# Kernel tuning notes

Measured on AMD Instinct MI355X. Metric: run time of the kernel, lower is better.

Reference implementation:

```python
import jax, jax.numpy as jnp
import numpy as np


def setup_inputs() -> dict:
    key = jax.random.key(0)
    ks = jax.random.split(key, 8)
    E = 2_000_000          # num facts (edges)
    B, M = 8, 2000         # batch, max_local_entity -> B*M = 16000 entity slots
    R, D = 2000, 128       # num relations, hidden size (in_features == out_features)
    return {
        "local_entity": jax.random.randint(ks[0], (B, M), 0, M),
        "batch_heads": jax.random.randint(ks[1], (E,), 0, B * M),
        "batch_tails": jax.random.randint(ks[2], (E,), 0, B * M),
        "batch_rels": jax.random.randint(ks[3], (E,), 0, R),
        "val_one": jax.random.uniform(ks[4], (E,), dtype=jnp.float32),
        "rel_features": jax.random.normal(ks[5], (R, D), dtype=jnp.float32),
        "W": jax.random.normal(ks[6], (D, D), dtype=jnp.float32) * 0.05,
        "b": jax.random.normal(ks[7], (D,), dtype=jnp.float32) * 0.05,
    }


def reference(local_entity, batch_heads, batch_tails, batch_rels, val_one,
              rel_features, W, b):
    B, M = local_entity.shape
    num_ent = B * M
    # gather relation features per fact, linear transform (nn.Linear: x @ W.T + b)
    fact_rel = rel_features[batch_rels]            # [E, D]
    fact_val = fact_rel @ W.T + b                  # [E, D]
    # sparse COO mm == weighted scatter-add of fact_val into entity slots
    weighted = fact_val * val_one[:, None]         # [E, D]
    tail_agg = jax.ops.segment_sum(weighted, batch_tails, num_segments=num_ent)
    head_agg = jax.ops.segment_sum(weighted, batch_heads, num_segments=num_ent)
    f2e_emb = jax.nn.relu(tail_agg + head_agg)     # [B*M, D]
    return f2e_emb.reshape(B, M, -1)
```

## Files before the change

kernel.cpp:

```cpp
#include <hip/hip_runtime.h>
#include <hip/hip_bf16.h>
#include <cstdint>

typedef _Float16 half2v __attribute__((ext_vector_type(2)));

#define EPB   16
#define MAXNB 1024
#define FPB   4096
#define FPT   16
#define SORTCAP 4608
#define CPT   9

__global__ void rwb_row_kernel(const float* __restrict__ rel, const float* __restrict__ W,
                               const float* __restrict__ b, _Float16* __restrict__ rwb,
                               int R) {
    const int k = blockIdx.x;
    const int n = threadIdx.x;
    __shared__ float relk[128];
    relk[n] = rel[(size_t)k * 128 + n];
    __syncthreads();
    const float4* w4 = reinterpret_cast<const float4*>(W + (size_t)n * 128);
    const float4* r4 = reinterpret_cast<const float4*>(relk);
    float acc = 0.f;
#pragma unroll
    for (int i = 0; i < 32; ++i) {
        float4 a = r4[i], w = w4[i];
        acc += a.x * w.x + a.y * w.y + a.z * w.z + a.w * w.w;
    }
    rwb[(size_t)k * 128 + n] = (_Float16)(acc + b[n]);
}

__device__ __noinline__ void spill_add(float* __restrict__ out, const _Float16* __restrict__ rwb,
                                       int v, int r, float val) {
    float* o = out + (size_t)v * 128;
    const _Float16* rw = rwb + (size_t)r * 128;
    for (int n = 0; n < 128; ++n) unsafeAtomicAdd(o + n, val * (float)rw[n]);
}

__global__ __launch_bounds__(256) void bin_kernel(
    const int* __restrict__ heads, const int* __restrict__ tails,
    const int* __restrict__ rels, const float* __restrict__ val,
    int* __restrict__ gcnt, uint2* __restrict__ slots,
    const _Float16* __restrict__ rwb, float* __restrict__ out,
    int E, int NB, int CAPB) {
    __shared__ int cnt[MAXNB];
    __shared__ int gbase[MAXNB];
    const int t = threadIdx.x;
    for (int k = t; k < NB; k += 256) cnt[k] = 0;
    __syncthreads();

    const int base = blockIdx.x * FPB;
    unsigned keyT[FPT], keyH[FPT], prT[FPT], prH[FPT];
    float fv[FPT];
#pragma unroll
    for (int u = 0; u < FPT; ++u) {
        const int i = base + u * 256 + t;
        prT[u] = 0xFFFFFFFFu;
        prH[u] = 0xFFFFFFFFu;
        if (i < E) {
            const int tl = tails[i], hd = heads[i], r = rels[i];
            fv[u] = val[i];
            const int bt = tl >> 4, bh = hd >> 4;
            keyT[u] = ((unsigned)(tl & 15) << 24) | (unsigned)r;
            keyH[u] = ((unsigned)(hd & 15) << 24) | (unsigned)r;
            const int rt = atomicAdd(&cnt[bt], 1);
            const int rh = atomicAdd(&cnt[bh], 1);
            prT[u] = ((unsigned)bt << 16) | (unsigned)rt;
            prH[u] = ((unsigned)bh << 16) | (unsigned)rh;
        }
    }
    __syncthreads();
    for (int k = t; k < NB; k += 256) {
        const int c = cnt[k];
        gbase[k] = c ? atomicAdd(&gcnt[k], c) : 0;
    }
    __syncthreads();
#pragma unroll
    for (int u = 0; u < FPT; ++u) {
        if (prT[u] != 0xFFFFFFFFu) {
            {
                const int b = (int)(prT[u] >> 16);
                const int pos = gbase[b] + (int)(prT[u] & 0xFFFFu);
                uint2 pk; pk.x = keyT[u]; pk.y = __float_as_uint(fv[u]);
                if (pos < CAPB) slots[(size_t)b * CAPB + pos] = pk;
                else spill_add(out, rwb, (b << 4) | (int)(keyT[u] >> 24),
                               (int)(keyT[u] & 0xFFFFFFu), fv[u]);
            }
            {
                const int b = (int)(prH[u] >> 16);
                const int pos = gbase[b] + (int)(prH[u] & 0xFFFFu);
                uint2 pk; pk.x = keyH[u]; pk.y = __float_as_uint(fv[u]);
                if (pos < CAPB) slots[(size_t)b * CAPB + pos] = pk;
                else spill_add(out, rwb, (b << 4) | (int)(keyH[u] >> 24),
                               (int)(keyH[u] & 0xFFFFFFu), fv[u]);
            }
        }
    }
}

__global__ __launch_bounds__(512) void gather_kernel(
    const uint2* __restrict__ slots, const int* __restrict__ gcnt,
    const _Float16* __restrict__ rwb, float* __restrict__ out,
    int NUMENT, int CAPB) {
    __shared__ uint2 se[SORTCAP];
    __shared__ int cnt[EPB], basep[EPB];
    const int t = threadIdx.x;
    const int b = blockIdx.x;
    if (t < EPB) cnt[t] = 0;
    __syncthreads();

    int deg = gcnt[b];
    if (deg > CAPB) deg = CAPB;
    const uint2* sl = slots + (size_t)b * CAPB;

    uint2 e[CPT];
    int rk[CPT];
#pragma unroll
    for (int u = 0; u < CPT; ++u) {
        const int k = t + u * 512;
        rk[u] = -1;
        if (k < deg) {
            e[u] = sl[k];
            rk[u] = atomicAdd(&cnt[(int)(e[u].x >> 24)], 1);
        }
    }
    __syncthreads();
    if (t == 0) {
        int s = 0;
#pragma unroll
        for (int i = 0; i < EPB; ++i) { basep[i] = s; s += cnt[i]; }
    }
    __syncthreads();
#pragma unroll
    for (int u = 0; u < CPT; ++u)
        if (rk[u] >= 0) se[basep[(int)(e[u].x >> 24)] + rk[u]] = e[u];
    __syncthreads();

    const int wv = t >> 6, lane = t & 63;
    const unsigned* rwb32 = reinterpret_cast<const unsigned*>(rwb);
#pragma unroll
    for (int ei = 0; ei < 2; ++ei) {
        const int le = wv * 2 + ei;
        const int vent = b * EPB + le;
        const int s0 = basep[le], c = cnt[le];
        float a0 = 0.f, a1 = 0.f;
        int j = 0;
        for (; j + 8 <= c; j += 8) {
            uint2 q[8];
#pragma unroll
            for (int u = 0; u < 8; ++u) q[u] = se[s0 + j + u];
            unsigned rw[8];
#pragma unroll
            for (int u = 0; u < 8; ++u)
                rw[u] = rwb32[(size_t)(q[u].x & 0xFFFFFFu) * 64 + lane];
#pragma unroll
            for (int u = 0; u < 8; ++u) {
                const float w = __uint_as_float(q[u].y);
                const half2v h = __builtin_bit_cast(half2v, rw[u]);
                a0 += w * (float)h[0];
                a1 += w * (float)h[1];
            }
        }
        for (; j < c; ++j) {
            const uint2 q = se[s0 + j];
            const float w = __uint_as_float(q.y);
            const unsigned rwv = rwb32[(size_t)(q.x & 0xFFFFFFu) * 64 + lane];
            const half2v h = __builtin_bit_cast(half2v, rwv);
            a0 += w * (float)h[0];
            a1 += w * (float)h[1];
        }
        if (vent < NUMENT) {
            float* op = out + (size_t)vent * 128 + 2 * lane;
            float2 sp = *reinterpret_cast<const float2*>(op);
            float2 o;
            o.x = fmaxf(a0 + sp.x, 0.f);
            o.y = fmaxf(a1 + sp.y, 0.f);
            *reinterpret_cast<float2*>(op) = o;
        }
    }
}

__global__ void rwb_f32_kernel(const float* __restrict__ rel, const float* __restrict__ W,
                               const float* __restrict__ b, float* __restrict__ rwb, int R) {
    const int k = blockIdx.x;
    const int n = threadIdx.x;
    __shared__ float relk[128];
    relk[n] = rel[(size_t)k * 128 + n];
    __syncthreads();
    const float4* w4 = reinterpret_cast<const float4*>(W + (size_t)n * 128);
    const float4* r4 = reinterpret_cast<const float4*>(relk);
    float acc = 0.f;
#pragma unroll
    for (int i = 0; i < 32; ++i) {
        float4 a = r4[i], w = w4[i];
        acc += a.x * w.x + a.y * w.y + a.z * w.z + a.w * w.w;
    }
    rwb[(size_t)k * 128 + n] = acc + b[n];
}

__global__ void scatter_vec_kernel(const int* __restrict__ heads, const int* __restrict__ tails,
                                   const int* __restrict__ rels, const float* __restrict__ val,
                                   const float* __restrict__ rwb, float* __restrict__ out,
                                   long long nitems) {
    const long long i = (long long)blockIdx.x * blockDim.x + threadIdx.x;
    if (i >= nitems) return;
    const int e = (int)(i >> 5);
    const int c = (int)(i & 31) * 4;
    const float v = val[e];
    float4 rw = *reinterpret_cast<const float4*>(rwb + (size_t)rels[e] * 128 + c);
    float* pt = out + (size_t)tails[e] * 128 + c;
    float* ph = out + (size_t)heads[e] * 128 + c;
    unsafeAtomicAdd(pt + 0, v * rw.x); unsafeAtomicAdd(pt + 1, v * rw.y);
    unsafeAtomicAdd(pt + 2, v * rw.z); unsafeAtomicAdd(pt + 3, v * rw.w);
    unsafeAtomicAdd(ph + 0, v * rw.x); unsafeAtomicAdd(ph + 1, v * rw.y);
    unsafeAtomicAdd(ph + 2, v * rw.z); unsafeAtomicAdd(ph + 3, v * rw.w);
}

__global__ void relu_kernel(float* __restrict__ out, int n4) {
    const int i = blockIdx.x * blockDim.x + threadIdx.x;
    if (i >= n4) return;
    float4* p = reinterpret_cast<float4*>(out) + i;
    float4 v = *p;
    v.x = fmaxf(v.x, 0.f); v.y = fmaxf(v.y, 0.f);
    v.z = fmaxf(v.z, 0.f); v.w = fmaxf(v.w, 0.f);
    *p = v;
}

extern "C" void kernel_launch(void* const* d_in, const int* in_sizes, int n_in,
                              void* d_out, int out_size, void* d_ws, size_t ws_size,
                              hipStream_t stream) {
    const int* heads = (const int*)d_in[1];
    const int* tails = (const int*)d_in[2];
    const int* rels  = (const int*)d_in[3];
    const float* val  = (const float*)d_in[4];
    const float* relf = (const float*)d_in[5];
    const float* W    = (const float*)d_in[6];
    const float* b    = (const float*)d_in[7];
    float* out = (float*)d_out;

    const int NUMENT = in_sizes[0];
    const int E      = in_sizes[1];
    const int D      = in_sizes[7];
    const int R      = in_sizes[5] / D;

    const int NB = (NUMENT + EPB - 1) / EPB;
    const long long mean = (2LL * E * EPB) / (NUMENT > 0 ? NUMENT : 1);
    int CAPB = (int)(mean + mean / 16 + 256);

    const size_t rwb_bytes = (size_t)R * D * sizeof(_Float16);
    const size_t off_gcnt  = (rwb_bytes + 255) & ~(size_t)255;
    const size_t gcnt_b    = (size_t)NB * sizeof(int);
    const size_t off_slots = (off_gcnt + gcnt_b + 255) & ~(size_t)255;
    const size_t slots_b   = (size_t)NB * CAPB * sizeof(uint2);

    if (NB <= MAXNB && R < (1 << 24) && CAPB <= SORTCAP &&
        ws_size >= off_slots + slots_b) {
        _Float16* rwb = (_Float16*)d_ws;
        int* gcnt     = (int*)((char*)d_ws + off_gcnt);
        uint2* slots  = (uint2*)((char*)d_ws + off_slots);

        hipMemsetAsync(gcnt, 0, gcnt_b, stream);
        hipMemsetAsync(out, 0, (size_t)out_size * sizeof(float), stream);
        rwb_row_kernel<<<R, 128, 0, stream>>>(relf, W, b, rwb, R);
        bin_kernel<<<(E + FPB - 1) / FPB, 256, 0, stream>>>(
            heads, tails, rels, val, gcnt, slots, rwb, out, E, NB, CAPB);
        gather_kernel<<<NB, 512, 0, stream>>>(slots, gcnt, rwb, out, NUMENT, CAPB);
    } else {
        float* rwb = (float*)d_ws;
        hipMemsetAsync(out, 0, (size_t)out_size * sizeof(float), stream);
        rwb_f32_kernel<<<R, 128, 0, stream>>>(relf, W, b, rwb, R);
        const long long items = (long long)E * 32;
        scatter_vec_kernel<<<(unsigned)((items + 255) / 256), 256, 0, stream>>>(
            heads, tails, rels, val, rwb, out, items);
        relu_kernel<<<(out_size / 4 + 255) / 256, 256, 0, stream>>>(out, out_size / 4);
    }
}
```

Measured before the change: 210.8 us.

## Pack binned fact entries into 32 bits with fp16 weight and 12-bit relation

Each binned fact entry shrinks from an 8-byte (key, fp32 weight) pair to one 32-bit word: a 4-bit local entity, a 12-bit relation id and an fp16 weight. This halves slot write and read traffic and the shared-memory sort footprint in the gather kernel. Separately, the bin kernel now uses 512 threads and 8192 facts per block. The weights lose precision to fp16, and the fast path now requires fewer than 4096 relations.

```diff
diff --git a/kernel.cpp b/kernel.cpp
--- a/kernel.cpp
+++ b/kernel.cpp
@@ -6,10 +6,15 @@
 
 #define EPB   16
 #define MAXNB 1024
-#define FPB   4096
+#define FPB   8192
 #define FPT   16
 #define SORTCAP 4608
 #define CPT   9
+
+
+__device__ __forceinline__ float pay_val(unsigned p) {
+    return (float)__builtin_bit_cast(_Float16, (unsigned short)(p & 0xFFFFu));
+}
 
 __global__ void rwb_row_kernel(const float* __restrict__ rel, const float* __restrict__ W,
                                const float* __restrict__ b, _Float16* __restrict__ rwb,
@@ -31,38 +36,40 @@
 }
 
 __device__ __noinline__ void spill_add(float* __restrict__ out, const _Float16* __restrict__ rwb,
-                                       int v, int r, float val) {
+                                       int v, unsigned pay) {
+    const int r = (int)((pay >> 16) & 0xFFFu);
+    const float val = pay_val(pay);
     float* o = out + (size_t)v * 128;
     const _Float16* rw = rwb + (size_t)r * 128;
     for (int n = 0; n < 128; ++n) unsafeAtomicAdd(o + n, val * (float)rw[n]);
 }
 
-__global__ __launch_bounds__(256) void bin_kernel(
+__global__ __launch_bounds__(512) void bin_kernel(
     const int* __restrict__ heads, const int* __restrict__ tails,
     const int* __restrict__ rels, const float* __restrict__ val,
-    int* __restrict__ gcnt, uint2* __restrict__ slots,
+    int* __restrict__ gcnt, unsigned* __restrict__ slots,
     const _Float16* __restrict__ rwb, float* __restrict__ out,
     int E, int NB, int CAPB) {
     __shared__ int cnt[MAXNB];
     __shared__ int gbase[MAXNB];
     const int t = threadIdx.x;
-    for (int k = t; k < NB; k += 256) cnt[k] = 0;
+    for (int k = t; k < NB; k += 512) cnt[k] = 0;
     __syncthreads();
 
     const int base = blockIdx.x * FPB;
-    unsigned keyT[FPT], keyH[FPT], prT[FPT], prH[FPT];
-    float fv[FPT];
+    unsigned payT[FPT], payH[FPT], prT[FPT], prH[FPT];
 #pragma unroll
     for (int u = 0; u < FPT; ++u) {
-        const int i = base + u * 256 + t;
+        const int i = base + u * 512 + t;
         prT[u] = 0xFFFFFFFFu;
         prH[u] = 0xFFFFFFFFu;
         if (i < E) {
             const int tl = tails[i], hd = heads[i], r = rels[i];
-            fv[u] = val[i];
+            const unsigned hv =
+                (unsigned)__builtin_bit_cast(unsigned short, (_Float16)val[i]);
             const int bt = tl >> 4, bh = hd >> 4;
-            keyT[u] = ((unsigned)(tl & 15) << 24) | (unsigned)r;
-            keyH[u] = ((unsigned)(hd & 15) << 24) | (unsigned)r;
+            payT[u] = ((unsigned)(tl & 15) << 28) | ((unsigned)r << 16) | hv;
+            payH[u] = ((unsigned)(hd & 15) << 28) | ((unsigned)r << 16) | hv;
             const int rt = atomicAdd(&cnt[bt], 1);
             const int rh = atomicAdd(&cnt[bh], 1);
             prT[u] = ((unsigned)bt << 16) | (unsigned)rt;
@@ -70,7 +77,7 @@
         }
     }
     __syncthreads();
-    for (int k = t; k < NB; k += 256) {
+    for (int k = t; k < NB; k += 512) {
         const int c = cnt[k];
         gbase[k] = c ? atomicAdd(&gcnt[k], c) : 0;
     }
@@ -79,30 +86,26 @@
     for (int u = 0; u < FPT; ++u) {
         if (prT[u] != 0xFFFFFFFFu) {
             {
-                const int b = (int)(prT[u] >> 16);
-                const int pos = gbase[b] + (int)(prT[u] & 0xFFFFu);
-                uint2 pk; pk.x = keyT[u]; pk.y = __float_as_uint(fv[u]);
-                if (pos < CAPB) slots[(size_t)b * CAPB + pos] = pk;
-                else spill_add(out, rwb, (b << 4) | (int)(keyT[u] >> 24),
-                               (int)(keyT[u] & 0xFFFFFFu), fv[u]);
+                const int b1 = (int)(prT[u] >> 16);
+                const int pos = gbase[b1] + (int)(prT[u] & 0xFFFFu);
+                if (pos < CAPB) slots[(size_t)b1 * CAPB + pos] = payT[u];
+                else spill_add(out, rwb, (b1 << 4) | (int)(payT[u] >> 28), payT[u]);
             }
             {
-                const int b = (int)(prH[u] >> 16);
-                const int pos = gbase[b] + (int)(prH[u] & 0xFFFFu);
-                uint2 pk; pk.x = keyH[u]; pk.y = __float_as_uint(fv[u]);
-                if (pos < CAPB) slots[(size_t)b * CAPB + pos] = pk;
-                else spill_add(out, rwb, (b << 4) | (int)(keyH[u] >> 24),
-                               (int)(keyH[u] & 0xFFFFFFu), fv[u]);
+                const int b1 = (int)(prH[u] >> 16);
+                const int pos = gbase[b1] + (int)(prH[u] & 0xFFFFu);
+                if (pos < CAPB) slots[(size_t)b1 * CAPB + pos] = payH[u];
+                else spill_add(out, rwb, (b1 << 4) | (int)(payH[u] >> 28), payH[u]);
             }
         }
     }
 }
 
 __global__ __launch_bounds__(512) void gather_kernel(
-    const uint2* __restrict__ slots, const int* __restrict__ gcnt,
+    const unsigned* __restrict__ slots, const int* __restrict__ gcnt,
     const _Float16* __restrict__ rwb, float* __restrict__ out,
     int NUMENT, int CAPB) {
-    __shared__ uint2 se[SORTCAP];
+    __shared__ unsigned se[SORTCAP];
     __shared__ int cnt[EPB], basep[EPB];
     const int t = threadIdx.x;
     const int b = blockIdx.x;
@@ -111,9 +114,9 @@
 
     int deg = gcnt[b];
     if (deg > CAPB) deg = CAPB;
-    const uint2* sl = slots + (size_t)b * CAPB;
-
-    uint2 e[CPT];
+    const unsigned* sl = slots + (size_t)b * CAPB;
+
+    unsigned e[CPT];
     int rk[CPT];
 #pragma unroll
     for (int u = 0; u < CPT; ++u) {
@@ -121,7 +124,7 @@
         rk[u] = -1;
         if (k < deg) {
             e[u] = sl[k];
-            rk[u] = atomicAdd(&cnt[(int)(e[u].x >> 24)], 1);
+            rk[u] = atomicAdd(&cnt[(int)(e[u] >> 28)], 1);
         }
     }
     __syncthreads();
@@ -133,7 +136,7 @@
     __syncthreads();
 #pragma unroll
     for (int u = 0; u < CPT; ++u)
-        if (rk[u] >= 0) se[basep[(int)(e[u].x >> 24)] + rk[u]] = e[u];
+        if (rk[u] >= 0) se[basep[(int)(e[u] >> 28)] + rk[u]] = e[u];
     __syncthreads();
 
     const int wv = t >> 6, lane = t & 63;
@@ -146,25 +149,25 @@
         float a0 = 0.f, a1 = 0.f;
         int j = 0;
         for (; j + 8 <= c; j += 8) {
-            uint2 q[8];
+            unsigned q[8];
 #pragma unroll
             for (int u = 0; u < 8; ++u) q[u] = se[s0 + j + u];
             unsigned rw[8];
 #pragma unroll
             for (int u = 0; u < 8; ++u)
-                rw[u] = rwb32[(size_t)(q[u].x & 0xFFFFFFu) * 64 + lane];
+                rw[u] = rwb32[(size_t)((q[u] >> 16) & 0xFFFu) * 64 + lane];
 #pragma unroll
             for (int u = 0; u < 8; ++u) {
-                const float w = __uint_as_float(q[u].y);
+                const float w = pay_val(q[u]);
                 const half2v h = __builtin_bit_cast(half2v, rw[u]);
                 a0 += w * (float)h[0];
                 a1 += w * (float)h[1];
             }
         }
         for (; j < c; ++j) {
-            const uint2 q = se[s0 + j];
-            const float w = __uint_as_float(q.y);
-            const unsigned rwv = rwb32[(size_t)(q.x & 0xFFFFFFu) * 64 + lane];
+            const unsigned q = se[s0 + j];
+            const float w = pay_val(q);
+            const unsigned rwv = rwb32[(size_t)((q >> 16) & 0xFFFu) * 64 + lane];
             const half2v h = __builtin_bit_cast(half2v, rwv);
             a0 += w * (float)h[0];
             a1 += w * (float)h[1];
@@ -251,18 +254,18 @@
     const size_t off_gcnt  = (rwb_bytes + 255) & ~(size_t)255;
     const size_t gcnt_b    = (size_t)NB * sizeof(int);
     const size_t off_slots = (off_gcnt + gcnt_b + 255) & ~(size_t)255;
-    const size_t slots_b   = (size_t)NB * CAPB * sizeof(uint2);
-
-    if (NB <= MAXNB && R < (1 << 24) && CAPB <= SORTCAP &&
+    const size_t slots_b   = (size_t)NB * CAPB * sizeof(unsigned);
+
+    if (NB <= MAXNB && R < 4096 && CAPB <= SORTCAP &&
         ws_size >= off_slots + slots_b) {
-        _Float16* rwb = (_Float16*)d_ws;
-        int* gcnt     = (int*)((char*)d_ws + off_gcnt);
-        uint2* slots  = (uint2*)((char*)d_ws + off_slots);
+        _Float16* rwb   = (_Float16*)d_ws;
+        int* gcnt       = (int*)((char*)d_ws + off_gcnt);
+        unsigned* slots = (unsigned*)((char*)d_ws + off_slots);
 
         hipMemsetAsync(gcnt, 0, gcnt_b, stream);
         hipMemsetAsync(out, 0, (size_t)out_size * sizeof(float), stream);
         rwb_row_kernel<<<R, 128, 0, stream>>>(relf, W, b, rwb, R);
-        bin_kernel<<<(E + FPB - 1) / FPB, 256, 0, stream>>>(
+        bin_kernel<<<(E + FPB - 1) / FPB, 512, 0, stream>>>(
             heads, tails, rels, val, gcnt, slots, rwb, out, E, NB, CAPB);
         gather_kernel<<<NB, 512, 0, stream>>>(slots, gcnt, rwb, out, NUMENT, CAPB);
     } else {
```

Result: no change. 208.7 us (-1.0%).
